# Performance work log

Hardware: AMD Instinct MI355X
Metric: run time of the kernel (lower is better)

Reference implementation:

```python
import jax, jax.numpy as jnp
import numpy as np

N_NODES = 50000
N_EDGES = 600000
LATENT = 128
IN_FEAT = 7
STEPS = 3
MLP_LAYERS = 2


def setup_inputs() -> dict:
    key = jax.random.key(0)
    ks = jax.random.split(key, 8)
    s = 0.05
    nodes = jax.random.normal(ks[0], (N_NODES, IN_FEAT), jnp.float32)
    senders = jax.random.randint(ks[1], (N_EDGES,), 0, N_NODES, jnp.int32)
    receivers = jax.random.randint(ks[2], (N_EDGES,), 0, N_NODES, jnp.int32)
    W_embed = jax.random.normal(ks[3], (IN_FEAT, LATENT), jnp.float32) * s
    b_embed = jnp.zeros((LATENT,), jnp.float32)
    mlp_W = jax.random.normal(ks[4], (STEPS, MLP_LAYERS, LATENT, LATENT), jnp.float32) * s
    mlp_b = jnp.zeros((STEPS, MLP_LAYERS, LATENT), jnp.float32)
    ln_scale = jnp.ones((STEPS, LATENT), jnp.float32)
    ln_bias = jnp.zeros((STEPS, LATENT), jnp.float32)
    W_dec = jax.random.normal(ks[5], (LATENT, IN_FEAT), jnp.float32) * s
    b_dec = jnp.zeros((IN_FEAT,), jnp.float32)
    return dict(nodes=nodes, senders=senders, receivers=receivers,
                W_embed=W_embed, b_embed=b_embed, mlp_W=mlp_W, mlp_b=mlp_b,
                ln_scale=ln_scale, ln_bias=ln_bias, W_dec=W_dec, b_dec=b_dec)


def _layer_norm(x, scale, bias, eps=1e-6):
    mu = jnp.mean(x, axis=-1, keepdims=True)
    var = jnp.var(x, axis=-1, keepdims=True)
    return (x - mu) * jax.lax.rsqrt(var + eps) * scale + bias


def reference(nodes, senders, receivers, W_embed, b_embed, mlp_W, mlp_b,
              ln_scale, ln_bias, W_dec, b_dec):
    n = nodes.shape[0]
    # symmetric normalization factors (jraph GraphConvolution default)
    ones = jnp.ones((senders.shape[0],), dtype=nodes.dtype)
    sender_deg = jax.ops.segment_sum(ones, senders, num_segments=n)
    receiver_deg = jax.ops.segment_sum(ones, receivers, num_segments=n)
    inv_sqrt_s = jax.lax.rsqrt(jnp.maximum(sender_deg, 1.0))[:, None]
    inv_sqrt_r = jax.lax.rsqrt(jnp.maximum(receiver_deg, 1.0))[:, None]

    # node embedder
    h = nodes @ W_embed + b_embed  # [N, LATENT]
    for step in range(mlp_W.shape[0]):
        # per-node MLP update (update_node_fn applied before aggregation)
        x = h
        for l in range(mlp_W.shape[1]):
            x = jax.nn.relu(x @ mlp_W[step, l] + mlp_b[step, l])
        # normalized gather -> scatter-sum aggregation
        x = x * inv_sqrt_s
        x = jax.ops.segment_sum(x[senders], receivers, num_segments=n)
        x = x * inv_sqrt_r
        # skip connection + layer norm
        h = _layer_norm(h + x, ln_scale[step], ln_bias[step])
    # decoder back to input feature size
    return h @ W_dec + b_dec  # [N, IN_FEAT]
```

## Files before the change

kernel.cpp:

```cpp
#include <hip/hip_runtime.h>

#define NN 50000
#define NE 600000
#define LAT 128
#define IN_F 7
#define CSR_W 64
#define HSTR 136

typedef __attribute__((ext_vector_type(8))) short bfrag;
typedef __attribute__((ext_vector_type(4))) float ffrag;

__device__ inline unsigned short f2bf(float f) {
    unsigned int u = __float_as_uint(f);
    return (unsigned short)((u + 0x7FFFu + ((u >> 16) & 1u)) >> 16);
}
__device__ inline float bf2f(unsigned int b) { return __uint_as_float(b << 16); }


__global__ void k_pack_w(const float* __restrict__ W, unsigned short* __restrict__ Wp,
                         int nmat) {
    int t = blockIdx.x * 256 + threadIdx.x;
    if (t >= nmat * 8 * 4 * 64) return;
    int lane = t & 63;
    int ks = (t >> 6) & 3;
    int nt = (t >> 8) & 7;
    int mat = t >> 11;
    int n = nt * 16 + (lane & 15);
    int k0 = ks * 32 + (lane >> 4) * 8;
    const float* src = W + (size_t)mat * LAT * LAT;
    unsigned long long lo = 0, hi = 0;
#pragma unroll
    for (int j = 0; j < 4; ++j)
        lo |= (unsigned long long)f2bf(src[(k0 + j) * LAT + n]) << (16 * j);
#pragma unroll
    for (int j = 0; j < 4; ++j)
        hi |= (unsigned long long)f2bf(src[(k0 + 4 + j) * LAT + n]) << (16 * j);
    unsigned long long* dst = (unsigned long long*)(Wp + (size_t)t * 8);
    dst[0] = lo; dst[1] = hi;
}


__global__ __launch_bounds__(256) void k_fused1(
    const int* __restrict__ s, const int* __restrict__ r,
    unsigned int* __restrict__ cnt, unsigned short* __restrict__ slot,
    const float* __restrict__ nodes, const float* __restrict__ We,
    const float* __restrict__ be,
    const unsigned short* __restrict__ W0p, const unsigned short* __restrict__ W1p,
    const float* __restrict__ b0, const float* __restrict__ b1,
    unsigned short* __restrict__ x, int build_blocks)
{
    __shared__ unsigned short hs[64][HSTR];
    int tid = threadIdx.x;

    if ((int)blockIdx.x < build_blocks) {
        int i = blockIdx.x * 256 + tid;
        if (i < NE) {
            int ss = s[i], rr = r[i];
            atomicAdd(&cnt[ss], 1u);
            unsigned int p = atomicAdd(&cnt[rr], 0x10000u) >> 16;
            if (p < CSR_W) slot[(size_t)rr * CSR_W + p] = (unsigned short)ss;
        }
        return;
    }

    int brow = ((int)blockIdx.x - build_blocks) * 64;
    int rows = NN - brow; if (rows > 64) rows = 64;

#pragma unroll
    for (int it = 0; it < 8; ++it) {
        int fi = it * 256 + tid;
        int rr = fi >> 5, cc = (fi & 31) << 2;
        if (rr < rows) {
            const float* nr = nodes + (size_t)(brow + rr) * IN_F;
            float o0 = be[cc], o1 = be[cc + 1], o2 = be[cc + 2], o3 = be[cc + 3];
#pragma unroll
            for (int k = 0; k < IN_F; ++k) {
                float nv = nr[k];
                const float* wk = We + k * LAT + cc;
                o0 += nv * wk[0]; o1 += nv * wk[1];
                o2 += nv * wk[2]; o3 += nv * wk[3];
            }
            unsigned long long pk = (unsigned long long)f2bf(o0)
                | ((unsigned long long)f2bf(o1) << 16)
                | ((unsigned long long)f2bf(o2) << 32)
                | ((unsigned long long)f2bf(o3) << 48);
            *(unsigned long long*)&hs[rr][cc] = pk;
        }
    }
    __syncthreads();

    int w = tid >> 6, lane = tid & 63;
    int mrow = w * 16 + (lane & 15);
    int koff = (lane >> 4) * 8;
    int ccol = lane & 15;
    int crow = w * 16 + (lane >> 4) * 4;

    float bia0[8], bia1[8];
#pragma unroll
    for (int nt = 0; nt < 8; ++nt) { bia0[nt] = b0[nt * 16 + ccol]; bia1[nt] = b1[nt * 16 + ccol]; }

    ffrag acc[8];
#pragma unroll
    for (int nt = 0; nt < 8; ++nt) acc[nt] = (ffrag)0.0f;
#pragma unroll
    for (int ks = 0; ks < 4; ++ks) {
        bfrag af = *(const bfrag*)&hs[mrow][ks * 32 + koff];
#pragma unroll
        for (int nt = 0; nt < 8; ++nt) {
            bfrag bf = *(const bfrag*)&W0p[(size_t)(((nt * 4) + ks) * 64 + lane) * 8];
            acc[nt] = __builtin_amdgcn_mfma_f32_16x16x32_bf16(af, bf, acc[nt], 0, 0, 0);
        }
    }
#pragma unroll
    for (int nt = 0; nt < 8; ++nt)
#pragma unroll
        for (int reg = 0; reg < 4; ++reg)
            hs[crow + reg][nt * 16 + ccol] = f2bf(fmaxf(acc[nt][reg] + bia0[nt], 0.f));
    __syncthreads();

#pragma unroll
    for (int nt = 0; nt < 8; ++nt) acc[nt] = (ffrag)0.0f;
#pragma unroll
    for (int ks = 0; ks < 4; ++ks) {
        bfrag af = *(const bfrag*)&hs[mrow][ks * 32 + koff];
#pragma unroll
        for (int nt = 0; nt < 8; ++nt) {
            bfrag bf = *(const bfrag*)&W1p[(size_t)(((nt * 4) + ks) * 64 + lane) * 8];
            acc[nt] = __builtin_amdgcn_mfma_f32_16x16x32_bf16(af, bf, acc[nt], 0, 0, 0);
        }
    }
    __syncthreads();
#pragma unroll
    for (int nt = 0; nt < 8; ++nt)
#pragma unroll
        for (int reg = 0; reg < 4; ++reg)
            hs[crow + reg][nt * 16 + ccol] = f2bf(fmaxf(acc[nt][reg] + bia1[nt], 0.f));
    __syncthreads();

#pragma unroll
    for (int it = 0; it < 8; ++it) {
        int fi = it * 256 + tid;
        int rr = fi >> 5, cc = (fi & 31) << 2;
        if (rr < rows)
            *(unsigned long long*)&x[(size_t)(brow + rr) * LAT + cc] =
                *(unsigned long long*)&hs[rr][cc];
    }
}


__global__ __launch_bounds__(256) void k_mlp2(
    const unsigned short* __restrict__ h,
    const unsigned short* __restrict__ W0p, const unsigned short* __restrict__ W1p,
    const float* __restrict__ b0, const float* __restrict__ b1,
    unsigned short* __restrict__ x, int M)
{
    __shared__ unsigned short hs[64][HSTR];
    int brow = blockIdx.x * 64;
    int tid = threadIdx.x;
    int rows = M - brow; if (rows > 64) rows = 64;

#pragma unroll
    for (int it = 0; it < 8; ++it) {
        int fi = it * 256 + tid;
        int rr = fi >> 5, cc = (fi & 31) << 2;
        if (rr < rows)
            *(unsigned long long*)&hs[rr][cc] =
                *(const unsigned long long*)&h[(size_t)(brow + rr) * LAT + cc];
    }
    __syncthreads();

    int w = tid >> 6, lane = tid & 63;
    int mrow = w * 16 + (lane & 15);
    int koff = (lane >> 4) * 8;
    int ccol = lane & 15;
    int crow = w * 16 + (lane >> 4) * 4;

    float bia0[8], bia1[8];
#pragma unroll
    for (int nt = 0; nt < 8; ++nt) { bia0[nt] = b0[nt * 16 + ccol]; bia1[nt] = b1[nt * 16 + ccol]; }

    ffrag acc[8];
#pragma unroll
    for (int nt = 0; nt < 8; ++nt) acc[nt] = (ffrag)0.0f;
#pragma unroll
    for (int ks = 0; ks < 4; ++ks) {
        bfrag af = *(const bfrag*)&hs[mrow][ks * 32 + koff];
#pragma unroll
        for (int nt = 0; nt < 8; ++nt) {
            bfrag bf = *(const bfrag*)&W0p[(size_t)(((nt * 4) + ks) * 64 + lane) * 8];
            acc[nt] = __builtin_amdgcn_mfma_f32_16x16x32_bf16(af, bf, acc[nt], 0, 0, 0);
        }
    }
#pragma unroll
    for (int nt = 0; nt < 8; ++nt)
#pragma unroll
        for (int reg = 0; reg < 4; ++reg)
            hs[crow + reg][nt * 16 + ccol] = f2bf(fmaxf(acc[nt][reg] + bia0[nt], 0.f));
    __syncthreads();

#pragma unroll
    for (int nt = 0; nt < 8; ++nt) acc[nt] = (ffrag)0.0f;
#pragma unroll
    for (int ks = 0; ks < 4; ++ks) {
        bfrag af = *(const bfrag*)&hs[mrow][ks * 32 + koff];
#pragma unroll
        for (int nt = 0; nt < 8; ++nt) {
            bfrag bf = *(const bfrag*)&W1p[(size_t)(((nt * 4) + ks) * 64 + lane) * 8];
            acc[nt] = __builtin_amdgcn_mfma_f32_16x16x32_bf16(af, bf, acc[nt], 0, 0, 0);
        }
    }
    __syncthreads();
#pragma unroll
    for (int nt = 0; nt < 8; ++nt)
#pragma unroll
        for (int reg = 0; reg < 4; ++reg)
            hs[crow + reg][nt * 16 + ccol] = f2bf(fmaxf(acc[nt][reg] + bia1[nt], 0.f));
    __syncthreads();

#pragma unroll
    for (int it = 0; it < 8; ++it) {
        int fi = it * 256 + tid;
        int rr = fi >> 5, cc = (fi & 31) << 2;
        if (rr < rows)
            *(unsigned long long*)&x[(size_t)(brow + rr) * LAT + cc] =
                *(unsigned long long*)&hs[rr][cc];
    }
}


__global__ __launch_bounds__(256) void k_agg(
    const unsigned short* __restrict__ x, unsigned short* __restrict__ h,
    const float* __restrict__ nodes, const float* __restrict__ We,
    const float* __restrict__ be,
    const unsigned int* __restrict__ cnt, const unsigned short* __restrict__ slot,
    const float* __restrict__ gamma, const float* __restrict__ beta,
    const float* __restrict__ Wd, const float* __restrict__ bd,
    float* __restrict__ outd, int mode)
{
    int lane = threadIdx.x & 63;
    int r = blockIdx.x * 4 + (threadIdx.x >> 6);
    if (r >= NN) return;

    int ct = (int)(cnt[r] >> 16);
    float ir = rsqrtf((float)(ct > 1 ? ct : 1));
    int c = ct > CSR_W ? CSR_W : ct;

    int myidx = 0; float myinv = 0.f;
    if (lane < c) {
        myidx = (int)slot[(size_t)r * CSR_W + lane];
        unsigned int ds = cnt[myidx] & 0xFFFFu;
        myinv = rsqrtf((float)(ds > 1 ? ds : 1));
    }

    int j0 = lane * 2;
    float ax0 = 0.f, ay0 = 0.f, ax1 = 0.f, ay1 = 0.f;
    float ax2 = 0.f, ay2 = 0.f, ax3 = 0.f, ay3 = 0.f;

    int e = 0;
    for (; e + 4 <= c; e += 4) {
        int s0 = __shfl(myidx, e);
        int s1 = __shfl(myidx, e + 1);
        int s2 = __shfl(myidx, e + 2);
        int s3 = __shfl(myidx, e + 3);
        float w0 = __shfl(myinv, e);
        float w1 = __shfl(myinv, e + 1);
        float w2 = __shfl(myinv, e + 2);
        float w3 = __shfl(myinv, e + 3);
        unsigned int v0 = *(const unsigned int*)&x[(size_t)s0 * LAT + j0];
        unsigned int v1 = *(const unsigned int*)&x[(size_t)s1 * LAT + j0];
        unsigned int v2 = *(const unsigned int*)&x[(size_t)s2 * LAT + j0];
        unsigned int v3 = *(const unsigned int*)&x[(size_t)s3 * LAT + j0];
        ax0 += bf2f(v0 & 0xFFFFu) * w0; ay0 += bf2f(v0 >> 16) * w0;
        ax1 += bf2f(v1 & 0xFFFFu) * w1; ay1 += bf2f(v1 >> 16) * w1;
        ax2 += bf2f(v2 & 0xFFFFu) * w2; ay2 += bf2f(v2 >> 16) * w2;
        ax3 += bf2f(v3 & 0xFFFFu) * w3; ay3 += bf2f(v3 >> 16) * w3;
    }
    for (; e < c; ++e) {
        int s0 = __shfl(myidx, e);
        float w0 = __shfl(myinv, e);
        unsigned int v0 = *(const unsigned int*)&x[(size_t)s0 * LAT + j0];
        ax0 += bf2f(v0 & 0xFFFFu) * w0; ay0 += bf2f(v0 >> 16) * w0;
    }

    float a0 = ((ax0 + ax1) + (ax2 + ax3)) * ir;
    float a1 = ((ay0 + ay1) + (ay2 + ay3)) * ir;

    float v0, v1;
    if (mode == 0) {
        float o0 = be[j0], o1 = be[j0 + 1];
#pragma unroll
        for (int k = 0; k < IN_F; ++k) {
            float nv = nodes[(size_t)r * IN_F + k];
            o0 += nv * We[k * LAT + j0];
            o1 += nv * We[k * LAT + j0 + 1];
        }
        v0 = o0 + a0; v1 = o1 + a1;
    } else {
        unsigned int hv = *(const unsigned int*)&h[(size_t)r * LAT + j0];
        v0 = bf2f(hv & 0xFFFFu) + a0;
        v1 = bf2f(hv >> 16) + a1;
    }

    float sum = v0 + v1, sq = v0 * v0 + v1 * v1;
#pragma unroll
    for (int m = 1; m <= 32; m <<= 1) {
        sum += __shfl_xor(sum, m);
        sq  += __shfl_xor(sq, m);
    }
    float mu = sum * (1.f / LAT);
    float rs = rsqrtf(sq * (1.f / LAT) - mu * mu + 1e-6f);

    float o0 = (v0 - mu) * rs * gamma[j0] + beta[j0];
    float o1 = (v1 - mu) * rs * gamma[j0 + 1] + beta[j0 + 1];

    if (mode < 2) {
        *(unsigned int*)&h[(size_t)r * LAT + j0] =
            (unsigned int)f2bf(o0) | ((unsigned int)f2bf(o1) << 16);
    } else {
        const float* wd0 = Wd + j0 * IN_F;
        const float* wd1 = Wd + (j0 + 1) * IN_F;
#pragma unroll
        for (int f = 0; f < IN_F; ++f) {
            float pv = o0 * wd0[f] + o1 * wd1[f];
#pragma unroll
            for (int m = 1; m <= 32; m <<= 1) pv += __shfl_xor(pv, m);
            if (lane == 0) outd[(size_t)r * IN_F + f] = pv + bd[f];
        }
    }
}


extern "C" void kernel_launch(void* const* d_in, const int* in_sizes, int n_in,
                              void* d_out, int out_size, void* d_ws, size_t ws_size,
                              hipStream_t stream)
{
    const float* nodes   = (const float*)d_in[0];
    const int*   senders = (const int*)d_in[1];
    const int*   recvs   = (const int*)d_in[2];
    const float* W_embed = (const float*)d_in[3];
    const float* b_embed = (const float*)d_in[4];
    const float* mlp_W   = (const float*)d_in[5];
    const float* mlp_b   = (const float*)d_in[6];
    const float* ln_s    = (const float*)d_in[7];
    const float* ln_b    = (const float*)d_in[8];
    const float* W_dec   = (const float*)d_in[9];
    const float* b_dec   = (const float*)d_in[10];
    float* out = (float*)d_out;

    char* p = (char*)d_ws;
    auto alloc = [&](size_t bytes) -> char* {
        char* q = p; p += (bytes + 255) & ~(size_t)255; return q;
    };
    unsigned short* h    = (unsigned short*)alloc((size_t)NN * LAT * 2);
    unsigned short* x    = (unsigned short*)alloc((size_t)NN * LAT * 2);
    unsigned short* Wp   = (unsigned short*)alloc((size_t)6 * LAT * LAT * 2);
    unsigned int* cnt    = (unsigned int*)alloc((size_t)NN * 4);
    unsigned short* slot = (unsigned short*)alloc((size_t)NN * CSR_W * 2);

    hipMemsetAsync(cnt, 0, (size_t)NN * 4, stream);
    k_pack_w<<<(6 * 8 * 4 * 64 + 255) / 256, 256, 0, stream>>>(mlp_W, Wp, 6);

    int build_blocks = (NE + 255) / 256;
    int mlp_blocks   = (NN + 63) / 64;
    int agg_blocks   = (NN + 3) / 4;

    const float* b0 = mlp_b;
    k_fused1<<<build_blocks + mlp_blocks, 256, 0, stream>>>(
        senders, recvs, cnt, slot, nodes, W_embed, b_embed,
        Wp, Wp + (size_t)LAT * LAT, b0, b0 + LAT, x, build_blocks);

    k_agg<<<agg_blocks, 256, 0, stream>>>(
        x, h, nodes, W_embed, b_embed, cnt, slot,
        ln_s, ln_b, nullptr, nullptr, nullptr, 0);

    k_mlp2<<<mlp_blocks, 256, 0, stream>>>(
        h, Wp + (size_t)2 * LAT * LAT, Wp + (size_t)3 * LAT * LAT,
        b0 + 2 * LAT, b0 + 3 * LAT, x, NN);
    k_agg<<<agg_blocks, 256, 0, stream>>>(
        x, h, nodes, W_embed, b_embed, cnt, slot,
        ln_s + LAT, ln_b + LAT, nullptr, nullptr, nullptr, 1);

    k_mlp2<<<mlp_blocks, 256, 0, stream>>>(
        h, Wp + (size_t)4 * LAT * LAT, Wp + (size_t)5 * LAT * LAT,
        b0 + 4 * LAT, b0 + 5 * LAT, x, NN);
    k_agg<<<agg_blocks, 256, 0, stream>>>(
        x, h, nodes, W_embed, b_embed, cnt, slot,
        ln_s + 2 * LAT, ln_b + 2 * LAT, W_dec, b_dec, out, 2);
}
```

Measured before the change: 319.1 us.

## Fold sender normalization into MLP epilogue, unroll gather by eight, fuse memset into prep

For steps 1 and 2 the per-sender inverse-sqrt degree scale moves into the second MLP kernel's epilogue. The aggregation kernel then no longer needs an indirect cnt lookup or weight shuffles per edge in those modes. The gather loop is unrolled to eight edges with more independent accumulators, giving more loads in flight. The cnt memset is folded into the weight-packing kernel to drop one launch. Trade-offs are more registers per thread and a duplicated code path per mode.

```diff
diff --git a/kernel.cpp b/kernel.cpp
--- a/kernel.cpp
+++ b/kernel.cpp
@@ -17,26 +17,28 @@
 __device__ inline float bf2f(unsigned int b) { return __uint_as_float(b << 16); }
 
 
-__global__ void k_pack_w(const float* __restrict__ W, unsigned short* __restrict__ Wp,
-                         int nmat) {
+__global__ void k_prep(const float* __restrict__ W, unsigned short* __restrict__ Wp,
+                       unsigned int* __restrict__ cnt) {
     int t = blockIdx.x * 256 + threadIdx.x;
-    if (t >= nmat * 8 * 4 * 64) return;
-    int lane = t & 63;
-    int ks = (t >> 6) & 3;
-    int nt = (t >> 8) & 7;
-    int mat = t >> 11;
-    int n = nt * 16 + (lane & 15);
-    int k0 = ks * 32 + (lane >> 4) * 8;
-    const float* src = W + (size_t)mat * LAT * LAT;
-    unsigned long long lo = 0, hi = 0;
-#pragma unroll
-    for (int j = 0; j < 4; ++j)
-        lo |= (unsigned long long)f2bf(src[(k0 + j) * LAT + n]) << (16 * j);
-#pragma unroll
-    for (int j = 0; j < 4; ++j)
-        hi |= (unsigned long long)f2bf(src[(k0 + 4 + j) * LAT + n]) << (16 * j);
-    unsigned long long* dst = (unsigned long long*)(Wp + (size_t)t * 8);
-    dst[0] = lo; dst[1] = hi;
+    if (t < NN) cnt[t] = 0;
+    if (t < 6 * 8 * 4 * 64) {
+        int lane = t & 63;
+        int ks = (t >> 6) & 3;
+        int nt = (t >> 8) & 7;
+        int mat = t >> 11;
+        int n = nt * 16 + (lane & 15);
+        int k0 = ks * 32 + (lane >> 4) * 8;
+        const float* src = W + (size_t)mat * LAT * LAT;
+        unsigned long long lo = 0, hi = 0;
+#pragma unroll
+        for (int j = 0; j < 4; ++j)
+            lo |= (unsigned long long)f2bf(src[(k0 + j) * LAT + n]) << (16 * j);
+#pragma unroll
+        for (int j = 0; j < 4; ++j)
+            hi |= (unsigned long long)f2bf(src[(k0 + 4 + j) * LAT + n]) << (16 * j);
+        unsigned long long* dst = (unsigned long long*)(Wp + (size_t)t * 8);
+        dst[0] = lo; dst[1] = hi;
+    }
 }
 
 
@@ -152,6 +154,7 @@
     const unsigned short* __restrict__ h,
     const unsigned short* __restrict__ W0p, const unsigned short* __restrict__ W1p,
     const float* __restrict__ b0, const float* __restrict__ b1,
+    const unsigned int* __restrict__ cnt,
     unsigned short* __restrict__ x, int M)
 {
     __shared__ unsigned short hs[64][HSTR];
@@ -178,6 +181,13 @@
     float bia0[8], bia1[8];
 #pragma unroll
     for (int nt = 0; nt < 8; ++nt) { bia0[nt] = b0[nt * 16 + ccol]; bia1[nt] = b1[nt * 16 + ccol]; }
+    float iv[4];
+#pragma unroll
+    for (int reg = 0; reg < 4; ++reg) {
+        int rw = brow + crow + reg;
+        unsigned int ds = cnt[rw < NN ? rw : NN - 1] & 0xFFFFu;
+        iv[reg] = rsqrtf((float)(ds > 1 ? ds : 1));
+    }
 
     ffrag acc[8];
 #pragma unroll
@@ -214,7 +224,8 @@
     for (int nt = 0; nt < 8; ++nt)
 #pragma unroll
         for (int reg = 0; reg < 4; ++reg)
-            hs[crow + reg][nt * 16 + ccol] = f2bf(fmaxf(acc[nt][reg] + bia1[nt], 0.f));
+            hs[crow + reg][nt * 16 + ccol] =
+                f2bf(fmaxf(acc[nt][reg] + bia1[nt], 0.f) * iv[reg]);
     __syncthreads();
 
 #pragma unroll
@@ -245,45 +256,111 @@
     float ir = rsqrtf((float)(ct > 1 ? ct : 1));
     int c = ct > CSR_W ? CSR_W : ct;
 
-    int myidx = 0; float myinv = 0.f;
-    if (lane < c) {
-        myidx = (int)slot[(size_t)r * CSR_W + lane];
-        unsigned int ds = cnt[myidx] & 0xFFFFu;
-        myinv = rsqrtf((float)(ds > 1 ? ds : 1));
-    }
+    int myidx = (lane < c) ? (int)slot[(size_t)r * CSR_W + lane] : 0;
 
     int j0 = lane * 2;
     float ax0 = 0.f, ay0 = 0.f, ax1 = 0.f, ay1 = 0.f;
     float ax2 = 0.f, ay2 = 0.f, ax3 = 0.f, ay3 = 0.f;
-
+    float ax4 = 0.f, ay4 = 0.f, ax5 = 0.f, ay5 = 0.f;
+    float ax6 = 0.f, ay6 = 0.f, ax7 = 0.f, ay7 = 0.f;
     int e = 0;
-    for (; e + 4 <= c; e += 4) {
-        int s0 = __shfl(myidx, e);
-        int s1 = __shfl(myidx, e + 1);
-        int s2 = __shfl(myidx, e + 2);
-        int s3 = __shfl(myidx, e + 3);
-        float w0 = __shfl(myinv, e);
-        float w1 = __shfl(myinv, e + 1);
-        float w2 = __shfl(myinv, e + 2);
-        float w3 = __shfl(myinv, e + 3);
-        unsigned int v0 = *(const unsigned int*)&x[(size_t)s0 * LAT + j0];
-        unsigned int v1 = *(const unsigned int*)&x[(size_t)s1 * LAT + j0];
-        unsigned int v2 = *(const unsigned int*)&x[(size_t)s2 * LAT + j0];
-        unsigned int v3 = *(const unsigned int*)&x[(size_t)s3 * LAT + j0];
-        ax0 += bf2f(v0 & 0xFFFFu) * w0; ay0 += bf2f(v0 >> 16) * w0;
-        ax1 += bf2f(v1 & 0xFFFFu) * w1; ay1 += bf2f(v1 >> 16) * w1;
-        ax2 += bf2f(v2 & 0xFFFFu) * w2; ay2 += bf2f(v2 >> 16) * w2;
-        ax3 += bf2f(v3 & 0xFFFFu) * w3; ay3 += bf2f(v3 >> 16) * w3;
-    }
-    for (; e < c; ++e) {
-        int s0 = __shfl(myidx, e);
-        float w0 = __shfl(myinv, e);
-        unsigned int v0 = *(const unsigned int*)&x[(size_t)s0 * LAT + j0];
-        ax0 += bf2f(v0 & 0xFFFFu) * w0; ay0 += bf2f(v0 >> 16) * w0;
-    }
-
-    float a0 = ((ax0 + ax1) + (ax2 + ax3)) * ir;
-    float a1 = ((ay0 + ay1) + (ay2 + ay3)) * ir;
+
+    if (mode == 0) {
+        float myinv = 0.f;
+        if (lane < c) {
+            unsigned int ds = cnt[myidx] & 0xFFFFu;
+            myinv = rsqrtf((float)(ds > 1 ? ds : 1));
+        }
+        for (; e + 8 <= c; e += 8) {
+            int s0 = __shfl(myidx, e),     s1 = __shfl(myidx, e + 1);
+            int s2 = __shfl(myidx, e + 2), s3 = __shfl(myidx, e + 3);
+            int s4 = __shfl(myidx, e + 4), s5 = __shfl(myidx, e + 5);
+            int s6 = __shfl(myidx, e + 6), s7 = __shfl(myidx, e + 7);
+            float w0 = __shfl(myinv, e),     w1 = __shfl(myinv, e + 1);
+            float w2 = __shfl(myinv, e + 2), w3 = __shfl(myinv, e + 3);
+            float w4 = __shfl(myinv, e + 4), w5 = __shfl(myinv, e + 5);
+            float w6 = __shfl(myinv, e + 6), w7 = __shfl(myinv, e + 7);
+            unsigned int v0 = *(const unsigned int*)&x[(size_t)s0 * LAT + j0];
+            unsigned int v1 = *(const unsigned int*)&x[(size_t)s1 * LAT + j0];
+            unsigned int v2 = *(const unsigned int*)&x[(size_t)s2 * LAT + j0];
+            unsigned int v3 = *(const unsigned int*)&x[(size_t)s3 * LAT + j0];
+            unsigned int v4 = *(const unsigned int*)&x[(size_t)s4 * LAT + j0];
+            unsigned int v5 = *(const unsigned int*)&x[(size_t)s5 * LAT + j0];
+            unsigned int v6 = *(const unsigned int*)&x[(size_t)s6 * LAT + j0];
+            unsigned int v7 = *(const unsigned int*)&x[(size_t)s7 * LAT + j0];
+            ax0 += bf2f(v0 & 0xFFFFu) * w0; ay0 += bf2f(v0 >> 16) * w0;
+            ax1 += bf2f(v1 & 0xFFFFu) * w1; ay1 += bf2f(v1 >> 16) * w1;
+            ax2 += bf2f(v2 & 0xFFFFu) * w2; ay2 += bf2f(v2 >> 16) * w2;
+            ax3 += bf2f(v3 & 0xFFFFu) * w3; ay3 += bf2f(v3 >> 16) * w3;
+            ax4 += bf2f(v4 & 0xFFFFu) * w4; ay4 += bf2f(v4 >> 16) * w4;
+            ax5 += bf2f(v5 & 0xFFFFu) * w5; ay5 += bf2f(v5 >> 16) * w5;
+            ax6 += bf2f(v6 & 0xFFFFu) * w6; ay6 += bf2f(v6 >> 16) * w6;
+            ax7 += bf2f(v7 & 0xFFFFu) * w7; ay7 += bf2f(v7 >> 16) * w7;
+        }
+        for (; e + 4 <= c; e += 4) {
+            int s0 = __shfl(myidx, e),     s1 = __shfl(myidx, e + 1);
+            int s2 = __shfl(myidx, e + 2), s3 = __shfl(myidx, e + 3);
+            float w0 = __shfl(myinv, e),     w1 = __shfl(myinv, e + 1);
+            float w2 = __shfl(myinv, e + 2), w3 = __shfl(myinv, e + 3);
+            unsigned int v0 = *(const unsigned int*)&x[(size_t)s0 * LAT + j0];
+            unsigned int v1 = *(const unsigned int*)&x[(size_t)s1 * LAT + j0];
+            unsigned int v2 = *(const unsigned int*)&x[(size_t)s2 * LAT + j0];
+            unsigned int v3 = *(const unsigned int*)&x[(size_t)s3 * LAT + j0];
+            ax0 += bf2f(v0 & 0xFFFFu) * w0; ay0 += bf2f(v0 >> 16) * w0;
+            ax1 += bf2f(v1 & 0xFFFFu) * w1; ay1 += bf2f(v1 >> 16) * w1;
+            ax2 += bf2f(v2 & 0xFFFFu) * w2; ay2 += bf2f(v2 >> 16) * w2;
+            ax3 += bf2f(v3 & 0xFFFFu) * w3; ay3 += bf2f(v3 >> 16) * w3;
+        }
+        for (; e < c; ++e) {
+            int s0 = __shfl(myidx, e);
+            float w0 = __shfl(myinv, e);
+            unsigned int v0 = *(const unsigned int*)&x[(size_t)s0 * LAT + j0];
+            ax0 += bf2f(v0 & 0xFFFFu) * w0; ay0 += bf2f(v0 >> 16) * w0;
+        }
+    } else {
+        for (; e + 8 <= c; e += 8) {
+            int s0 = __shfl(myidx, e),     s1 = __shfl(myidx, e + 1);
+            int s2 = __shfl(myidx, e + 2), s3 = __shfl(myidx, e + 3);
+            int s4 = __shfl(myidx, e + 4), s5 = __shfl(myidx, e + 5);
+            int s6 = __shfl(myidx, e + 6), s7 = __shfl(myidx, e + 7);
+            unsigned int v0 = *(const unsigned int*)&x[(size_t)s0 * LAT + j0];
+            unsigned int v1 = *(const unsigned int*)&x[(size_t)s1 * LAT + j0];
+            unsigned int v2 = *(const unsigned int*)&x[(size_t)s2 * LAT + j0];
+            unsigned int v3 = *(const unsigned int*)&x[(size_t)s3 * LAT + j0];
+            unsigned int v4 = *(const unsigned int*)&x[(size_t)s4 * LAT + j0];
+            unsigned int v5 = *(const unsigned int*)&x[(size_t)s5 * LAT + j0];
+            unsigned int v6 = *(const unsigned int*)&x[(size_t)s6 * LAT + j0];
+            unsigned int v7 = *(const unsigned int*)&x[(size_t)s7 * LAT + j0];
+            ax0 += bf2f(v0 & 0xFFFFu); ay0 += bf2f(v0 >> 16);
+            ax1 += bf2f(v1 & 0xFFFFu); ay1 += bf2f(v1 >> 16);
+            ax2 += bf2f(v2 & 0xFFFFu); ay2 += bf2f(v2 >> 16);
+            ax3 += bf2f(v3 & 0xFFFFu); ay3 += bf2f(v3 >> 16);
+            ax4 += bf2f(v4 & 0xFFFFu); ay4 += bf2f(v4 >> 16);
+            ax5 += bf2f(v5 & 0xFFFFu); ay5 += bf2f(v5 >> 16);
+            ax6 += bf2f(v6 & 0xFFFFu); ay6 += bf2f(v6 >> 16);
+            ax7 += bf2f(v7 & 0xFFFFu); ay7 += bf2f(v7 >> 16);
+        }
+        for (; e + 4 <= c; e += 4) {
+            int s0 = __shfl(myidx, e),     s1 = __shfl(myidx, e + 1);
+            int s2 = __shfl(myidx, e + 2), s3 = __shfl(myidx, e + 3);
+            unsigned int v0 = *(const unsigned int*)&x[(size_t)s0 * LAT + j0];
+            unsigned int v1 = *(const unsigned int*)&x[(size_t)s1 * LAT + j0];
+            unsigned int v2 = *(const unsigned int*)&x[(size_t)s2 * LAT + j0];
+            unsigned int v3 = *(const unsigned int*)&x[(size_t)s3 * LAT + j0];
+            ax0 += bf2f(v0 & 0xFFFFu); ay0 += bf2f(v0 >> 16);
+            ax1 += bf2f(v1 & 0xFFFFu); ay1 += bf2f(v1 >> 16);
+            ax2 += bf2f(v2 & 0xFFFFu); ay2 += bf2f(v2 >> 16);
+            ax3 += bf2f(v3 & 0xFFFFu); ay3 += bf2f(v3 >> 16);
+        }
+        for (; e < c; ++e) {
+            int s0 = __shfl(myidx, e);
+            unsigned int v0 = *(const unsigned int*)&x[(size_t)s0 * LAT + j0];
+            ax0 += bf2f(v0 & 0xFFFFu); ay0 += bf2f(v0 >> 16);
+        }
+    }
+
+    float a0 = (((ax0 + ax1) + (ax2 + ax3)) + ((ax4 + ax5) + (ax6 + ax7))) * ir;
+    float a1 = (((ay0 + ay1) + (ay2 + ay3)) + ((ay4 + ay5) + (ay6 + ay7))) * ir;
 
     float v0, v1;
     if (mode == 0) {
@@ -357,8 +434,7 @@
     unsigned int* cnt    = (unsigned int*)alloc((size_t)NN * 4);
     unsigned short* slot = (unsigned short*)alloc((size_t)NN * CSR_W * 2);
 
-    hipMemsetAsync(cnt, 0, (size_t)NN * 4, stream);
-    k_pack_w<<<(6 * 8 * 4 * 64 + 255) / 256, 256, 0, stream>>>(mlp_W, Wp, 6);
+    k_prep<<<(NN + 255) / 256, 256, 0, stream>>>(mlp_W, Wp, cnt);
 
     int build_blocks = (NE + 255) / 256;
     int mlp_blocks   = (NN + 63) / 64;
@@ -375,14 +451,14 @@
 
     k_mlp2<<<mlp_blocks, 256, 0, stream>>>(
         h, Wp + (size_t)2 * LAT * LAT, Wp + (size_t)3 * LAT * LAT,
-        b0 + 2 * LAT, b0 + 3 * LAT, x, NN);
+        b0 + 2 * LAT, b0 + 3 * LAT, cnt, x, NN);
     k_agg<<<agg_blocks, 256, 0, stream>>>(
         x, h, nodes, W_embed, b_embed, cnt, slot,
         ln_s + LAT, ln_b + LAT, nullptr, nullptr, nullptr, 1);
 
     k_mlp2<<<mlp_blocks, 256, 0, stream>>>(
         h, Wp + (size_t)4 * LAT * LAT, Wp + (size_t)5 * LAT * LAT,
-        b0 + 4 * LAT, b0 + 5 * LAT, x, NN);
+        b0 + 4 * LAT, b0 + 5 * LAT, cnt, x, NN);
     k_agg<<<agg_blocks, 256, 0, stream>>>(
         x, h, nodes, W_embed, b_embed, cnt, slot,
         ln_s + 2 * LAT, ln_b + 2 * LAT, W_dec, b_dec, out, 2);
```

Measured after the change: 319.0 us. Within noise of the previous version (-0.0%).
